# Kernel tuning notes

Measured on AMD Instinct MI355X. Metric: run time of the kernel, lower is better.

The kernel has to match this reference:

```python
import jax, jax.numpy as jnp
import numpy as np

N_QUBITS = 8
N_CYCLES = 4
N_LAYERS = 2  # log2(8) - 1
B = 65536

CNOT = jnp.array([[1, 0, 0, 0],
                  [0, 1, 0, 0],
                  [0, 0, 0, 1],
                  [0, 0, 1, 0]], dtype=jnp.complex64)


def apply_gate(state, U, wires):
    """Apply a (2^k x 2^k) gate U on the given wires of state (B, 2,2,...,2).
    Wire 0 is the leftmost (most significant) qubit axis."""
    k = len(wires)
    src = [w + 1 for w in wires]
    dst = list(range(1, 1 + k))
    st = jnp.moveaxis(state, src, dst)
    shp = st.shape
    st = st.reshape(shp[0], 2 ** k, -1)
    st = jnp.einsum('ij,bjr->bir', U, st)
    return jnp.moveaxis(st.reshape(shp), dst, src)


def apply_ry(state, q, angles):
    """Batched RY(angle) on qubit q; angles has shape (B,)."""
    st = jnp.moveaxis(state, q + 1, 1)  # (B, 2, rest...)
    c = jnp.cos(0.5 * angles).reshape((-1,) + (1,) * (st.ndim - 2))
    s = jnp.sin(0.5 * angles).reshape((-1,) + (1,) * (st.ndim - 2))
    s0, s1 = st[:, 0], st[:, 1]
    new = jnp.stack([c * s0 - s * s1, s * s0 + c * s1], axis=1)
    return jnp.moveaxis(new, 1, q + 1)


def crx_mat(theta):
    c = (jnp.cos(0.5 * theta) + 0j).astype(jnp.complex64)
    s = (-1j * jnp.sin(0.5 * theta)).astype(jnp.complex64)
    one = jnp.ones((), jnp.complex64)
    zero = jnp.zeros((), jnp.complex64)
    return jnp.stack([
        jnp.stack([one, zero, zero, zero]),
        jnp.stack([zero, one, zero, zero]),
        jnp.stack([zero, zero, c, s]),
        jnp.stack([zero, zero, s, c]),
    ])


def u3_mat(p):
    th, ph, lm = p[0], p[1], p[2]
    ct = (jnp.cos(0.5 * th) + 0j).astype(jnp.complex64)
    st = (jnp.sin(0.5 * th) + 0j).astype(jnp.complex64)
    el = jnp.exp(1j * lm).astype(jnp.complex64)
    ep = jnp.exp(1j * ph).astype(jnp.complex64)
    return jnp.stack([
        jnp.stack([ct, -el * st]),
        jnp.stack([ep * st, ep * el * ct]),
    ])


def expval_z(state, q):
    st = jnp.moveaxis(state, q + 1, 1)
    p = (st.real ** 2 + st.imag ** 2).reshape(st.shape[0], 2, -1).sum(-1)
    return p[:, 0] - p[:, 1]


def _forward(x, crx_theta, u3_params, w1, b1, w2, b2):
    b = x.shape[0]
    # |0...0> initial state, shape (B, 2,2,...,2)
    state = jnp.zeros((b, 2 ** N_QUBITS), jnp.complex64).at[:, 0].set(1.0)
    state = state.reshape((b,) + (2,) * N_QUBITS)
    # encoder: data re-uploading RY angle encoding + CNOT ring, n_cycles times
    for _ in range(N_CYCLES):
        for q in range(N_QUBITS):
            state = apply_ry(state, q, x[:, q])
        for q in range(N_QUBITS):
            state = apply_gate(state, CNOT, [q, (q + 1) % N_QUBITS])
    # QCNN conv/pool layers with shared weights per layer
    active = list(range(N_QUBITS))
    for layer in range(N_LAYERS):
        U = crx_mat(crx_theta[layer])
        for i in range(0, len(active) - 1, 2):
            state = apply_gate(state, U, [active[i], active[i + 1]])
        for i in range(1, len(active) - 1, 2):
            state = apply_gate(state, U, [active[i], active[i + 1]])
        remain = active[1::2]
        # mid-circuit expval in the original is discarded and does not alter state
        V = u3_mat(u3_params[layer])
        for q in remain:
            state = apply_gate(state, V, [q])
        active = remain
    feats = jnp.stack([expval_z(state, q) for q in active], axis=1)  # (B, 2)
    h = jnp.tanh(feats @ w1 + b1)
    return jax.nn.sigmoid(h @ w2 + b2)  # (B, 1)


def setup_inputs() -> dict:
    key = jax.random.key(0)
    ks = jax.random.split(key, 6)
    return {
        'x': jax.random.normal(ks[0], (B, N_QUBITS), jnp.float32),
        'crx_theta': jax.random.normal(ks[1], (N_LAYERS,), jnp.float32),
        'u3_params': jax.random.normal(ks[2], (N_LAYERS, 3), jnp.float32),
        'w1': jax.random.normal(ks[3], (2, 10), jnp.float32) * 0.5,
        'b1': jnp.zeros((10,), jnp.float32),
        'w2': jax.random.normal(ks[4], (10, 1), jnp.float32) * 0.5,
        'b2': jnp.zeros((1,), jnp.float32),
    }


def reference(x, crx_theta, u3_params, w1, b1, w2, b2):
    return _forward(x, crx_theta, u3_params, w1, b1, w2, b2)
```

## Files before the change

kernel.cpp:

```cpp
#include <hip/hip_runtime.h>


#define NQ 8

template<int M>
__device__ __forceinline__ float sx(float v) {
    if constexpr (M == 32) return __shfl_xor(v, 32, 64);
    else return __int_as_float(__builtin_amdgcn_ds_swizzle(
                 __float_as_int(v), (M << 10) | 0x1F));
}

__device__ __forceinline__ float bperm(int byte_addr, float v) {
    return __int_as_float(__builtin_amdgcn_ds_bpermute(byte_addr, __float_as_int(v)));
}

#define RY_L(q, M) do { \
    float o0 = sx<M>(a0), o1 = sx<M>(a1), o2 = sx<M>(a2), o3 = sx<M>(a3); \
    a0 = fmaf(c[q], a0, ts[q]*o0); a1 = fmaf(c[q], a1, ts[q]*o1); \
    a2 = fmaf(c[q], a2, ts[q]*o2); a3 = fmaf(c[q], a3, ts[q]*o3); \
} while(0)

#define CNOT_FUSED() do { \
    float t0 = pb ? a2 : a0, t1 = pb ? a3 : a1, t2 = pb ? a1 : a3, t3 = pb ? a0 : a2; \
    a0 = bperm(ba0, t0); a2 = bperm(ba0, t2); \
    a1 = bperm(ba1, t1); a3 = bperm(ba1, t3); \
} while(0)

#define SHFL8(M) \
    float ro0=sx<M>(re0), io0=sx<M>(im0), ro1=sx<M>(re1), io1=sx<M>(im1), \
          ro2=sx<M>(re2), io2=sx<M>(im2), ro3=sx<M>(re3), io3=sx<M>(im3);

#define CRX_LL(CSH, M, cc, sn) do { \
    const bool ct = (l >> (CSH)) & 1; \
    SHFL8(M) \
    if (ct) { \
        re0 = cc*re0 + sn*io0; im0 = cc*im0 - sn*ro0; \
        re1 = cc*re1 + sn*io1; im1 = cc*im1 - sn*ro1; \
        re2 = cc*re2 + sn*io2; im2 = cc*im2 - sn*ro2; \
        re3 = cc*re3 + sn*io3; im3 = cc*im3 - sn*ro3; \
    } \
} while(0)

#define CRX_FIRST_LL(CSH, M, cc, sn) do { \
    const bool ct = (l >> (CSH)) & 1; \
    float ro0 = sx<M>(re0), ro1 = sx<M>(re1), ro2 = sx<M>(re2), ro3 = sx<M>(re3); \
    if (ct) { \
        im0 = -sn*ro0; re0 = cc*re0; \
        im1 = -sn*ro1; re1 = cc*re1; \
        im2 = -sn*ro2; re2 = cc*re2; \
        im3 = -sn*ro3; re3 = cc*re3; \
    } \
} while(0)

#define RYC0(M, T) do { \
    SHFL8(M) \
    re0 = fmaf(uct0, re0, (T)*ro0); im0 = fmaf(uct0, im0, (T)*io0); \
    re1 = fmaf(uct0, re1, (T)*ro1); im1 = fmaf(uct0, im1, (T)*io1); \
    re2 = fmaf(uct0, re2, (T)*ro2); im2 = fmaf(uct0, im2, (T)*io2); \
    re3 = fmaf(uct0, re3, (T)*ro3); im3 = fmaf(uct0, im3, (T)*io3); \
} while(0)

#define DIAG4(CA, SA, CB, SB) do { float r_; \
    r_ = (CA)*re0 - (SA)*im0; im0 = fmaf((CA), im0, (SA)*re0); re0 = r_; \
    r_ = (CB)*re1 - (SB)*im1; im1 = fmaf((CB), im1, (SB)*re1); re1 = r_; \
    r_ = (CA)*re2 - (SA)*im2; im2 = fmaf((CA), im2, (SA)*re2); re2 = r_; \
    r_ = (CB)*re3 - (SB)*im3; im3 = fmaf((CB), im3, (SB)*re3); re3 = r_; \
} while(0)

#define U3D_LANE(SH, M, UCT, UST, CL, SL, CP, SP) do { \
    const bool b = (l >> (SH)) & 1; \
    if (b) { \
        float r; \
        r = CL*re0 - SL*im0; im0 = CL*im0 + SL*re0; re0 = r; \
        r = CL*re1 - SL*im1; im1 = CL*im1 + SL*re1; re1 = r; \
        r = CL*re2 - SL*im2; im2 = CL*im2 + SL*re2; re2 = r; \
        r = CL*re3 - SL*im3; im3 = CL*im3 + SL*re3; re3 = r; \
    } \
    { \
        const float t = b ? (UST) : -(UST); \
        SHFL8(M) \
        re0 = fmaf(UCT, re0, t*ro0); im0 = fmaf(UCT, im0, t*io0); \
        re1 = fmaf(UCT, re1, t*ro1); im1 = fmaf(UCT, im1, t*io1); \
        re2 = fmaf(UCT, re2, t*ro2); im2 = fmaf(UCT, im2, t*io2); \
        re3 = fmaf(UCT, re3, t*ro3); im3 = fmaf(UCT, im3, t*io3); \
    } \
    if (b) { \
        float r; \
        r = CP*re0 - SP*im0; im0 = CP*im0 + SP*re0; re0 = r; \
        r = CP*re1 - SP*im1; im1 = CP*im1 + SP*re1; re1 = r; \
        r = CP*re2 - SP*im2; im2 = CP*im2 + SP*re2; re2 = r; \
        r = CP*re3 - SP*im3; im3 = CP*im3 + SP*re3; re3 = r; \
    } \
} while(0)

#define U3_Q7(CTR, M01R, M01I, M10R, M10I, M11R, M11I) do { \
    float nr0 = CTR*re0 + M01R*re1 - M01I*im1; \
    float ni0 = CTR*im0 + M01R*im1 + M01I*re1; \
    float nr1 = M10R*re0 - M10I*im0 + M11R*re1 - M11I*im1; \
    float ni1 = M10R*im0 + M10I*re0 + M11R*im1 + M11I*re1; \
    float nr2 = CTR*re2 + M01R*re3 - M01I*im3; \
    float ni2 = CTR*im2 + M01R*im3 + M01I*re3; \
    float nr3 = M10R*re2 - M10I*im2 + M11R*re3 - M11I*im3; \
    float ni3 = M10R*im2 + M10I*re2 + M11R*im3 + M11I*re3; \
    re0 = nr0; im0 = ni0; re1 = nr1; im1 = ni1; \
    re2 = nr2; im2 = ni2; re3 = nr3; im3 = ni3; \
} while(0)

__global__ void qcnn_prep(const float* __restrict__ crx,
                          const float* __restrict__ u3p,
                          float* __restrict__ ws) {
    if (threadIdx.x == 0 && blockIdx.x == 0) {
        float sc0, cc0, sc1, cc1;
        __sincosf(0.5f * crx[0], &sc0, &cc0);
        __sincosf(0.5f * crx[1], &sc1, &cc1);
        ws[0] = cc0; ws[1] = sc0; ws[2] = cc1; ws[3] = sc1;
        {
            float th = u3p[0], ph = u3p[1], lm = u3p[2];
            float st_, ct_;
            __sincosf(0.5f * th, &st_, &ct_);
            ws[4] = ct_; ws[5] = st_; ws[6] = lm; ws[7] = ph;
        }
        {
            float th = u3p[3], ph = u3p[4], lm = u3p[5];
            float st_, ct_, sl, cl, sp, cp, spl, cpl;
            __sincosf(0.5f * th, &st_, &ct_);
            __sincosf(lm, &sl, &cl);
            __sincosf(ph, &sp, &cp);
            __sincosf(ph + lm, &spl, &cpl);
            ws[8] = ct_;  ws[9] = st_;  ws[10] = cl; ws[11] = sl; ws[12] = cp; ws[13] = sp;
            ws[14] = -st_ * cl;  ws[15] = -st_ * sl;
            ws[16] =  st_ * cp;  ws[17] =  st_ * sp;
            ws[18] =  ct_ * cpl; ws[19] =  ct_ * spl;
        }
    }
}

__global__ __launch_bounds__(256) void qcnn_kernel(
    const float* __restrict__ x,
    const float* __restrict__ ws,
    const float* __restrict__ w1,
    const float* __restrict__ b1,
    const float* __restrict__ w2,
    const float* __restrict__ b2,
    float* __restrict__ out,
    int Btot)
{
    const int gtid = blockIdx.x * blockDim.x + threadIdx.x;
    const int wave = gtid >> 6;
    const int l = threadIdx.x & 63;
    if (wave >= Btot) return;

    const bool pb = __builtin_popcount(l) & 1;
    const int addr0 = (l & 32) | ((l ^ (l >> 1)) & 31);
    const int ba0 = addr0 << 2;
    const int ba1 = ba0 ^ (48 << 2);

    const float4* xv = (const float4*)(x + wave * NQ);
    float4 xa = xv[0], xb = xv[1];
    float c[NQ], s[NQ], ts[6];
    {
        float ang[NQ] = {xa.x, xa.y, xa.z, xa.w, xb.x, xb.y, xb.z, xb.w};
#pragma unroll
        for (int q = 0; q < NQ; ++q) __sincosf(0.5f * ang[q], &s[q], &c[q]);
#pragma unroll
        for (int q = 0; q < 6; ++q) ts[q] = ((l >> (5 - q)) & 1) ? s[q] : -s[q];
    }

    const float crc0 = ws[0], crs0 = ws[1], crc1 = ws[2], crs1 = ws[3];
    const float uct0 = ws[4], ust0 = ws[5], lm0 = ws[6], ph0 = ws[7];
    const float uct1 = ws[8],  ust1 = ws[9],  cl1 = ws[10], sl1 = ws[11], cp1 = ws[12], sp1 = ws[13];
    const float u01r1 = ws[14], u01i1 = ws[15], u10r1 = ws[16], u10i1 = ws[17], u11r1 = ws[18], u11i1 = ws[19];

    const float kf = (float)(((l >> 4) & 1) + ((l >> 2) & 1) + (l & 1));
    float sA0, cA0, sB0, cB0, sA1, cA1, sB1, cB1;
    __sincosf(kf * lm0,          &sA0, &cA0);
    __sincosf((kf + 1.f) * lm0,  &sB0, &cB0);
    __sincosf(kf * ph0,          &sA1, &cA1);
    __sincosf((kf + 1.f) * ph0,  &sB1, &cB1);
    const float tu1 = ((l >> 4) & 1) ? ust0 : -ust0;
    const float tu3 = ((l >> 2) & 1) ? ust0 : -ust0;
    const float tu5 = (l & 1)        ? ust0 : -ust0;

    float a0, a1, a2, a3;
    {
        float pl = (((l >> 5) & 1) ? s[0] : c[0]);
        pl *= (((l >> 4) & 1) ? s[1] : c[1]);
        pl *= (((l >> 3) & 1) ? s[2] : c[2]);
        pl *= (((l >> 2) & 1) ? s[3] : c[3]);
        pl *= (((l >> 1) & 1) ? s[4] : c[4]);
        pl *= ((l & 1) ? s[5] : c[5]);
        float pc6 = pl * c[6], ps6 = pl * s[6];
        a0 = pc6 * c[7]; a1 = pc6 * s[7];
        a2 = ps6 * c[7]; a3 = ps6 * s[7];
    }
    CNOT_FUSED();
#pragma unroll
    for (int cyc = 0; cyc < 3; ++cyc) {
        RY_L(0, 32); RY_L(1, 16); RY_L(2, 8); RY_L(3, 4); RY_L(4, 2); RY_L(5, 1);
        {
            float n0 = c[6]*a0 - s[6]*a2, n1 = c[6]*a1 - s[6]*a3;
            float n2 = s[6]*a0 + c[6]*a2, n3 = s[6]*a1 + c[6]*a3;
            a0 = n0; a1 = n1; a2 = n2; a3 = n3;
        }
        {
            float n0 = c[7]*a0 - s[7]*a1, n1 = s[7]*a0 + c[7]*a1;
            float n2 = c[7]*a2 - s[7]*a3, n3 = s[7]*a2 + c[7]*a3;
            a0 = n0; a1 = n1; a2 = n2; a3 = n3;
        }
        CNOT_FUSED();
    }

    float re0 = a0, re1 = a1, re2 = a2, re3 = a3;
    float im0 = 0.f, im1 = 0.f, im2 = 0.f, im3 = 0.f;

    CRX_FIRST_LL(5, 16, crc0, crs0);
    CRX_LL(3, 4,  crc0, crs0);
    CRX_LL(1, 1,  crc0, crs0);
    {
        float nr2 = crc0*re2 + crs0*im3, ni2 = crc0*im2 - crs0*re3;
        float nr3 = crc0*re3 + crs0*im2, ni3 = crc0*im3 - crs0*re2;
        re2 = nr2; im2 = ni2; re3 = nr3; im3 = ni3;
    }
    CRX_LL(4, 8, crc0, crs0);
    CRX_LL(2, 2, crc0, crs0);
    {
        if (l & 1) {
            float nr0 = crc0*re0 + crs0*im2, ni0 = crc0*im0 - crs0*re2;
            float nr2 = crc0*re2 + crs0*im0, ni2 = crc0*im2 - crs0*re0;
            float nr1 = crc0*re1 + crs0*im3, ni1 = crc0*im1 - crs0*re3;
            float nr3 = crc0*re3 + crs0*im1, ni3 = crc0*im3 - crs0*re1;
            re0 = nr0; im0 = ni0; re1 = nr1; im1 = ni1;
            re2 = nr2; im2 = ni2; re3 = nr3; im3 = ni3;
        }
    }
    DIAG4(cA0, sA0, cB0, sB0);
    RYC0(16, tu1);
    RYC0(4,  tu3);
    RYC0(1,  tu5);
    {
        float nr0 = uct0*re0 - ust0*re1, ni0 = uct0*im0 - ust0*im1;
        float nr1 = ust0*re0 + uct0*re1, ni1 = ust0*im0 + uct0*im1;
        float nr2 = uct0*re2 - ust0*re3, ni2 = uct0*im2 - ust0*im3;
        float nr3 = ust0*re2 + uct0*re3, ni3 = ust0*im2 + uct0*im3;
        re0 = nr0; im0 = ni0; re1 = nr1; im1 = ni1;
        re2 = nr2; im2 = ni2; re3 = nr3; im3 = ni3;
    }
    DIAG4(cA1, sA1, cB1, sB1);

    CRX_LL(4, 4, crc1, crs1);
    {
        if (l & 1) {
            float nr0 = crc1*re0 + crs1*im1, ni0 = crc1*im0 - crs1*re1;
            float nr1 = crc1*re1 + crs1*im0, ni1 = crc1*im1 - crs1*re0;
            float nr2 = crc1*re2 + crs1*im3, ni2 = crc1*im2 - crs1*re3;
            float nr3 = crc1*re3 + crs1*im2, ni3 = crc1*im3 - crs1*re2;
            re0 = nr0; im0 = ni0; re1 = nr1; im1 = ni1;
            re2 = nr2; im2 = ni2; re3 = nr3; im3 = ni3;
        }
    }
    CRX_LL(2, 1, crc1, crs1);
    U3D_LANE(2, 4, uct1, ust1, cl1, sl1, cp1, sp1);
    U3_Q7(uct1, u01r1, u01i1, u10r1, u10i1, u11r1, u11i1);

    float n0 = re0*re0 + im0*im0;
    float n1 = re1*re1 + im1*im1;
    float n2 = re2*re2 + im2*im2;
    float n3 = re3*re3 + im3*im3;
    float f0 = (((l >> 2) & 1) ? -1.0f : 1.0f) * (n0 + n1 + n2 + n3);
    float f1 = (n0 - n1) + (n2 - n3);
    f0 += sx<1>(f0);  f1 += sx<1>(f1);
    f0 += sx<2>(f0);  f1 += sx<2>(f1);
    f0 += sx<4>(f0);  f1 += sx<4>(f1);
    f0 += sx<8>(f0);  f1 += sx<8>(f1);
    f0 += sx<16>(f0); f1 += sx<16>(f1);
    f0 += sx<32>(f0); f1 += sx<32>(f1);

    const int k = l & 15;
    float contrib = 0.0f;
    if (k < 10) {
        float z = fmaf(f0, w1[k], fmaf(f1, w1[10 + k], b1[k]));
        float e = __expf(2.0f * z);
        float h = (e - 1.0f) / (e + 1.0f);
        contrib = h * w2[k];
    }
    contrib += sx<1>(contrib);
    contrib += sx<2>(contrib);
    contrib += sx<4>(contrib);
    contrib += sx<8>(contrib);
    if (l == 0) {
        float a = contrib + b2[0];
        out[wave] = 1.0f / (1.0f + __expf(-a));
    }
}

extern "C" void kernel_launch(void* const* d_in, const int* in_sizes, int n_in,
                              void* d_out, int out_size, void* d_ws, size_t ws_size,
                              hipStream_t stream) {
    const float* x   = (const float*)d_in[0];
    const float* crx = (const float*)d_in[1];
    const float* u3p = (const float*)d_in[2];
    const float* w1  = (const float*)d_in[3];
    const float* b1  = (const float*)d_in[4];
    const float* w2  = (const float*)d_in[5];
    const float* b2  = (const float*)d_in[6];
    float* out = (float*)d_out;
    float* ws  = (float*)d_ws;

    const int B = in_sizes[0] / NQ;
    hipLaunchKernelGGL(qcnn_prep, dim3(1), dim3(64), 0, stream, crx, u3p, ws);
    const int wavesPerBlock = 256 / 64;
    const int grid = (B + wavesPerBlock - 1) / wavesPerBlock;
    hipLaunchKernelGGL(qcnn_kernel, dim3(grid), dim3(256), 0, stream,
                       x, ws, w1, b1, w2, b2, out, B);
}
```

Measured before the change: 142.0 us.

## Vectorize state arithmetic with packed float2 FMAs and precompute phase table

Rewrites the per-lane amplitude math to use two-wide float vectors so the compiler can emit packed FP32 instructions (v_pk_fma_f32) on CDNA, roughly halving ALU instruction count for gate updates. Separately, moves the per-lane sincos of phase multiples into the prep kernel as a small table indexed by lane popcount, replacing four sincos per lane with two vector loads. Shuffles remain scalar; packed code may add register moves or swizzle overhead for the vector swaps.

```diff
diff --git a/kernel.cpp b/kernel.cpp
--- a/kernel.cpp
+++ b/kernel.cpp
@@ -2,6 +2,12 @@
 
 
 #define NQ 8
+
+typedef float v2 __attribute__((ext_vector_type(2)));
+
+__device__ __forceinline__ v2 sp(float x) { return (v2){x, x}; }
+__device__ __forceinline__ v2 fma2(v2 a, v2 b, v2 c) { return __builtin_elementwise_fma(a, b, c); }
+__device__ __forceinline__ v2 swp(v2 v) { return __builtin_shufflevector(v, v, 1, 0); }
 
 template<int M>
 __device__ __forceinline__ float sx(float v) {
@@ -9,101 +15,42 @@
     else return __int_as_float(__builtin_amdgcn_ds_swizzle(
                  __float_as_int(v), (M << 10) | 0x1F));
 }
-
+template<int M>
+__device__ __forceinline__ v2 sx2(v2 v) {
+    v2 r; r.x = sx<M>(v.x); r.y = sx<M>(v.y); return r;
+}
 __device__ __forceinline__ float bperm(int byte_addr, float v) {
     return __int_as_float(__builtin_amdgcn_ds_bpermute(byte_addr, __float_as_int(v)));
 }
 
 #define RY_L(q, M) do { \
-    float o0 = sx<M>(a0), o1 = sx<M>(a1), o2 = sx<M>(a2), o3 = sx<M>(a3); \
-    a0 = fmaf(c[q], a0, ts[q]*o0); a1 = fmaf(c[q], a1, ts[q]*o1); \
-    a2 = fmaf(c[q], a2, ts[q]*o2); a3 = fmaf(c[q], a3, ts[q]*o3); \
+    v2 oA = sx2<M>(A), oB = sx2<M>(B); \
+    A = fma2(sp(c[q]), A, sp(ts[q]) * oA); \
+    B = fma2(sp(c[q]), B, sp(ts[q]) * oB); \
 } while(0)
 
 #define CNOT_FUSED() do { \
-    float t0 = pb ? a2 : a0, t1 = pb ? a3 : a1, t2 = pb ? a1 : a3, t3 = pb ? a0 : a2; \
-    a0 = bperm(ba0, t0); a2 = bperm(ba0, t2); \
-    a1 = bperm(ba1, t1); a3 = bperm(ba1, t3); \
+    v2 TA = pb ? B : A; \
+    v2 TS = pb ? A : B; \
+    A = (v2){ bperm(ba0, TA.x), bperm(ba1, TA.y) }; \
+    B = (v2){ bperm(ba0, TS.y), bperm(ba1, TS.x) }; \
 } while(0)
-
-#define SHFL8(M) \
-    float ro0=sx<M>(re0), io0=sx<M>(im0), ro1=sx<M>(re1), io1=sx<M>(im1), \
-          ro2=sx<M>(re2), io2=sx<M>(im2), ro3=sx<M>(re3), io3=sx<M>(im3);
 
 #define CRX_LL(CSH, M, cc, sn) do { \
     const bool ct = (l >> (CSH)) & 1; \
-    SHFL8(M) \
+    v2 oRa = sx2<M>(Ra), oIa = sx2<M>(Ia), oRb = sx2<M>(Rb), oIb = sx2<M>(Ib); \
     if (ct) { \
-        re0 = cc*re0 + sn*io0; im0 = cc*im0 - sn*ro0; \
-        re1 = cc*re1 + sn*io1; im1 = cc*im1 - sn*ro1; \
-        re2 = cc*re2 + sn*io2; im2 = cc*im2 - sn*ro2; \
-        re3 = cc*re3 + sn*io3; im3 = cc*im3 - sn*ro3; \
+        Ra = fma2(sp(cc), Ra, sp(sn)  * oIa); \
+        Ia = fma2(sp(cc), Ia, sp(-(sn)) * oRa); \
+        Rb = fma2(sp(cc), Rb, sp(sn)  * oIb); \
+        Ib = fma2(sp(cc), Ib, sp(-(sn)) * oRb); \
     } \
 } while(0)
 
-#define CRX_FIRST_LL(CSH, M, cc, sn) do { \
-    const bool ct = (l >> (CSH)) & 1; \
-    float ro0 = sx<M>(re0), ro1 = sx<M>(re1), ro2 = sx<M>(re2), ro3 = sx<M>(re3); \
-    if (ct) { \
-        im0 = -sn*ro0; re0 = cc*re0; \
-        im1 = -sn*ro1; re1 = cc*re1; \
-        im2 = -sn*ro2; re2 = cc*re2; \
-        im3 = -sn*ro3; re3 = cc*re3; \
-    } \
-} while(0)
-
 #define RYC0(M, T) do { \
-    SHFL8(M) \
-    re0 = fmaf(uct0, re0, (T)*ro0); im0 = fmaf(uct0, im0, (T)*io0); \
-    re1 = fmaf(uct0, re1, (T)*ro1); im1 = fmaf(uct0, im1, (T)*io1); \
-    re2 = fmaf(uct0, re2, (T)*ro2); im2 = fmaf(uct0, im2, (T)*io2); \
-    re3 = fmaf(uct0, re3, (T)*ro3); im3 = fmaf(uct0, im3, (T)*io3); \
-} while(0)
-
-#define DIAG4(CA, SA, CB, SB) do { float r_; \
-    r_ = (CA)*re0 - (SA)*im0; im0 = fmaf((CA), im0, (SA)*re0); re0 = r_; \
-    r_ = (CB)*re1 - (SB)*im1; im1 = fmaf((CB), im1, (SB)*re1); re1 = r_; \
-    r_ = (CA)*re2 - (SA)*im2; im2 = fmaf((CA), im2, (SA)*re2); re2 = r_; \
-    r_ = (CB)*re3 - (SB)*im3; im3 = fmaf((CB), im3, (SB)*re3); re3 = r_; \
-} while(0)
-
-#define U3D_LANE(SH, M, UCT, UST, CL, SL, CP, SP) do { \
-    const bool b = (l >> (SH)) & 1; \
-    if (b) { \
-        float r; \
-        r = CL*re0 - SL*im0; im0 = CL*im0 + SL*re0; re0 = r; \
-        r = CL*re1 - SL*im1; im1 = CL*im1 + SL*re1; re1 = r; \
-        r = CL*re2 - SL*im2; im2 = CL*im2 + SL*re2; re2 = r; \
-        r = CL*re3 - SL*im3; im3 = CL*im3 + SL*re3; re3 = r; \
-    } \
-    { \
-        const float t = b ? (UST) : -(UST); \
-        SHFL8(M) \
-        re0 = fmaf(UCT, re0, t*ro0); im0 = fmaf(UCT, im0, t*io0); \
-        re1 = fmaf(UCT, re1, t*ro1); im1 = fmaf(UCT, im1, t*io1); \
-        re2 = fmaf(UCT, re2, t*ro2); im2 = fmaf(UCT, im2, t*io2); \
-        re3 = fmaf(UCT, re3, t*ro3); im3 = fmaf(UCT, im3, t*io3); \
-    } \
-    if (b) { \
-        float r; \
-        r = CP*re0 - SP*im0; im0 = CP*im0 + SP*re0; re0 = r; \
-        r = CP*re1 - SP*im1; im1 = CP*im1 + SP*re1; re1 = r; \
-        r = CP*re2 - SP*im2; im2 = CP*im2 + SP*re2; re2 = r; \
-        r = CP*re3 - SP*im3; im3 = CP*im3 + SP*re3; re3 = r; \
-    } \
-} while(0)
-
-#define U3_Q7(CTR, M01R, M01I, M10R, M10I, M11R, M11I) do { \
-    float nr0 = CTR*re0 + M01R*re1 - M01I*im1; \
-    float ni0 = CTR*im0 + M01R*im1 + M01I*re1; \
-    float nr1 = M10R*re0 - M10I*im0 + M11R*re1 - M11I*im1; \
-    float ni1 = M10R*im0 + M10I*re0 + M11R*im1 + M11I*re1; \
-    float nr2 = CTR*re2 + M01R*re3 - M01I*im3; \
-    float ni2 = CTR*im2 + M01R*im3 + M01I*re3; \
-    float nr3 = M10R*re2 - M10I*im2 + M11R*re3 - M11I*im3; \
-    float ni3 = M10R*im2 + M10I*re2 + M11R*im3 + M11I*re3; \
-    re0 = nr0; im0 = ni0; re1 = nr1; im1 = ni1; \
-    re2 = nr2; im2 = ni2; re3 = nr3; im3 = ni3; \
+    v2 oRa = sx2<M>(Ra), oIa = sx2<M>(Ia), oRb = sx2<M>(Rb), oIb = sx2<M>(Ib); \
+    Ra = fma2(sp(uct0), Ra, sp(T) * oRa); Ia = fma2(sp(uct0), Ia, sp(T) * oIa); \
+    Rb = fma2(sp(uct0), Rb, sp(T) * oRb); Ib = fma2(sp(uct0), Ib, sp(T) * oIb); \
 } while(0)
 
 __global__ void qcnn_prep(const float* __restrict__ crx,
@@ -114,23 +61,35 @@
         __sincosf(0.5f * crx[0], &sc0, &cc0);
         __sincosf(0.5f * crx[1], &sc1, &cc1);
         ws[0] = cc0; ws[1] = sc0; ws[2] = cc1; ws[3] = sc1;
+        float lm0, ph0;
         {
-            float th = u3p[0], ph = u3p[1], lm = u3p[2];
+            float th = u3p[0]; ph0 = u3p[1]; lm0 = u3p[2];
             float st_, ct_;
             __sincosf(0.5f * th, &st_, &ct_);
-            ws[4] = ct_; ws[5] = st_; ws[6] = lm; ws[7] = ph;
+            ws[4] = ct_; ws[5] = st_;
         }
         {
             float th = u3p[3], ph = u3p[4], lm = u3p[5];
-            float st_, ct_, sl, cl, sp, cp, spl, cpl;
+            float st_, ct_, sl, cl, sp_, cp, spl, cpl;
             __sincosf(0.5f * th, &st_, &ct_);
             __sincosf(lm, &sl, &cl);
-            __sincosf(ph, &sp, &cp);
+            __sincosf(ph, &sp_, &cp);
             __sincosf(ph + lm, &spl, &cpl);
-            ws[8] = ct_;  ws[9] = st_;  ws[10] = cl; ws[11] = sl; ws[12] = cp; ws[13] = sp;
+            ws[8] = ct_;  ws[9] = st_;  ws[10] = cl; ws[11] = sl; ws[12] = cp; ws[13] = sp_;
             ws[14] = -st_ * cl;  ws[15] = -st_ * sl;
-            ws[16] =  st_ * cp;  ws[17] =  st_ * sp;
+            ws[16] =  st_ * cp;  ws[17] =  st_ * sp_;
             ws[18] =  ct_ * cpl; ws[19] =  ct_ * spl;
+        }
+        for (int k = 0; k < 4; ++k) {
+            float kf = (float)k;
+            float sA0, cA0, sB0, cB0, sA1, cA1, sB1, cB1;
+            __sincosf(kf * lm0,         &sA0, &cA0);
+            __sincosf((kf + 1.f) * lm0, &sB0, &cB0);
+            __sincosf(kf * ph0,         &sA1, &cA1);
+            __sincosf((kf + 1.f) * ph0, &sB1, &cB1);
+            float* q = ws + 20 + k * 8;
+            q[0] = cA0; q[1] = sA0; q[2] = cB0; q[3] = sB0;
+            q[4] = cA1; q[5] = sA1; q[6] = cB1; q[7] = sB1;
         }
     }
 }
@@ -167,21 +126,20 @@
     }
 
     const float crc0 = ws[0], crs0 = ws[1], crc1 = ws[2], crs1 = ws[3];
-    const float uct0 = ws[4], ust0 = ws[5], lm0 = ws[6], ph0 = ws[7];
+    const float uct0 = ws[4], ust0 = ws[5];
     const float uct1 = ws[8],  ust1 = ws[9],  cl1 = ws[10], sl1 = ws[11], cp1 = ws[12], sp1 = ws[13];
     const float u01r1 = ws[14], u01i1 = ws[15], u10r1 = ws[16], u10i1 = ws[17], u11r1 = ws[18], u11i1 = ws[19];
 
-    const float kf = (float)(((l >> 4) & 1) + ((l >> 2) & 1) + (l & 1));
-    float sA0, cA0, sB0, cB0, sA1, cA1, sB1, cB1;
-    __sincosf(kf * lm0,          &sA0, &cA0);
-    __sincosf((kf + 1.f) * lm0,  &sB0, &cB0);
-    __sincosf(kf * ph0,          &sA1, &cA1);
-    __sincosf((kf + 1.f) * ph0,  &sB1, &cB1);
+    const int ki = ((l >> 4) & 1) + ((l >> 2) & 1) + (l & 1);
+    const float4* dtab = (const float4*)(ws + 20 + ki * 8);
+    float4 d0 = dtab[0], d1 = dtab[1];
+    const v2 CAB_lm = {d0.x, d0.z}, SAB_lm = {d0.y, d0.w};
+    const v2 CAB_ph = {d1.x, d1.z}, SAB_ph = {d1.y, d1.w};
     const float tu1 = ((l >> 4) & 1) ? ust0 : -ust0;
     const float tu3 = ((l >> 2) & 1) ? ust0 : -ust0;
     const float tu5 = (l & 1)        ? ust0 : -ust0;
 
-    float a0, a1, a2, a3;
+    v2 A, B;
     {
         float pl = (((l >> 5) & 1) ? s[0] : c[0]);
         pl *= (((l >> 4) & 1) ? s[1] : c[1]);
@@ -189,96 +147,136 @@
         pl *= (((l >> 2) & 1) ? s[3] : c[3]);
         pl *= (((l >> 1) & 1) ? s[4] : c[4]);
         pl *= ((l & 1) ? s[5] : c[5]);
-        float pc6 = pl * c[6], ps6 = pl * s[6];
-        a0 = pc6 * c[7]; a1 = pc6 * s[7];
-        a2 = ps6 * c[7]; a3 = ps6 * s[7];
+        v2 cs7 = {c[7], s[7]};
+        A = sp(pl * c[6]) * cs7;
+        B = sp(pl * s[6]) * cs7;
     }
     CNOT_FUSED();
 #pragma unroll
     for (int cyc = 0; cyc < 3; ++cyc) {
         RY_L(0, 32); RY_L(1, 16); RY_L(2, 8); RY_L(3, 4); RY_L(4, 2); RY_L(5, 1);
         {
-            float n0 = c[6]*a0 - s[6]*a2, n1 = c[6]*a1 - s[6]*a3;
-            float n2 = s[6]*a0 + c[6]*a2, n3 = s[6]*a1 + c[6]*a3;
-            a0 = n0; a1 = n1; a2 = n2; a3 = n3;
+            v2 nA = fma2(sp(-s[6]), B, sp(c[6]) * A);
+            B = fma2(sp(c[6]), B, sp(s[6]) * A);
+            A = nA;
         }
         {
-            float n0 = c[7]*a0 - s[7]*a1, n1 = s[7]*a0 + c[7]*a1;
-            float n2 = c[7]*a2 - s[7]*a3, n3 = s[7]*a2 + c[7]*a3;
-            a0 = n0; a1 = n1; a2 = n2; a3 = n3;
+            v2 sv = {-s[7], s[7]};
+            A = fma2(sp(c[7]), A, sv * swp(A));
+            B = fma2(sp(c[7]), B, sv * swp(B));
         }
         CNOT_FUSED();
     }
 
-    float re0 = a0, re1 = a1, re2 = a2, re3 = a3;
-    float im0 = 0.f, im1 = 0.f, im2 = 0.f, im3 = 0.f;
-
-    CRX_FIRST_LL(5, 16, crc0, crs0);
-    CRX_LL(3, 4,  crc0, crs0);
-    CRX_LL(1, 1,  crc0, crs0);
-    {
-        float nr2 = crc0*re2 + crs0*im3, ni2 = crc0*im2 - crs0*re3;
-        float nr3 = crc0*re3 + crs0*im2, ni3 = crc0*im3 - crs0*re2;
-        re2 = nr2; im2 = ni2; re3 = nr3; im3 = ni3;
+    v2 Ra = A, Rb = B, Ia = sp(0.f), Ib = sp(0.f);
+
+    {
+        const bool ct = (l >> 5) & 1;
+        v2 oRa = sx2<16>(Ra), oRb = sx2<16>(Rb);
+        if (ct) {
+            Ia = sp(-crs0) * oRa; Ra = sp(crc0) * Ra;
+            Ib = sp(-crs0) * oRb; Rb = sp(crc0) * Rb;
+        }
+    }
+    CRX_LL(3, 4, crc0, crs0);
+    CRX_LL(1, 1, crc0, crs0);
+    {
+        v2 nRb = fma2(sp(crc0), Rb, sp(crs0) * swp(Ib));
+        Ib = fma2(sp(crc0), Ib, sp(-crs0) * swp(Rb));
+        Rb = nRb;
     }
     CRX_LL(4, 8, crc0, crs0);
     CRX_LL(2, 2, crc0, crs0);
     {
         if (l & 1) {
-            float nr0 = crc0*re0 + crs0*im2, ni0 = crc0*im0 - crs0*re2;
-            float nr2 = crc0*re2 + crs0*im0, ni2 = crc0*im2 - crs0*re0;
-            float nr1 = crc0*re1 + crs0*im3, ni1 = crc0*im1 - crs0*re3;
-            float nr3 = crc0*re3 + crs0*im1, ni3 = crc0*im3 - crs0*re1;
-            re0 = nr0; im0 = ni0; re1 = nr1; im1 = ni1;
-            re2 = nr2; im2 = ni2; re3 = nr3; im3 = ni3;
-        }
-    }
-    DIAG4(cA0, sA0, cB0, sB0);
+            v2 nRa = fma2(sp(crc0), Ra, sp(crs0) * Ib);
+            v2 nRb = fma2(sp(crc0), Rb, sp(crs0) * Ia);
+            v2 nIa = fma2(sp(crc0), Ia, sp(-crs0) * Rb);
+            v2 nIb = fma2(sp(crc0), Ib, sp(-crs0) * Ra);
+            Ra = nRa; Rb = nRb; Ia = nIa; Ib = nIb;
+        }
+    }
+    {
+        v2 nRa = fma2(CAB_lm, Ra, -SAB_lm * Ia);
+        Ia = fma2(CAB_lm, Ia, SAB_lm * Ra); Ra = nRa;
+        v2 nRb = fma2(CAB_lm, Rb, -SAB_lm * Ib);
+        Ib = fma2(CAB_lm, Ib, SAB_lm * Rb); Rb = nRb;
+    }
     RYC0(16, tu1);
     RYC0(4,  tu3);
     RYC0(1,  tu5);
     {
-        float nr0 = uct0*re0 - ust0*re1, ni0 = uct0*im0 - ust0*im1;
-        float nr1 = ust0*re0 + uct0*re1, ni1 = ust0*im0 + uct0*im1;
-        float nr2 = uct0*re2 - ust0*re3, ni2 = uct0*im2 - ust0*im3;
-        float nr3 = ust0*re2 + uct0*re3, ni3 = ust0*im2 + uct0*im3;
-        re0 = nr0; im0 = ni0; re1 = nr1; im1 = ni1;
-        re2 = nr2; im2 = ni2; re3 = nr3; im3 = ni3;
-    }
-    DIAG4(cA1, sA1, cB1, sB1);
+        v2 usv = {-ust0, ust0};
+        Ra = fma2(sp(uct0), Ra, usv * swp(Ra));
+        Rb = fma2(sp(uct0), Rb, usv * swp(Rb));
+        Ia = fma2(sp(uct0), Ia, usv * swp(Ia));
+        Ib = fma2(sp(uct0), Ib, usv * swp(Ib));
+    }
+    {
+        v2 nRa = fma2(CAB_ph, Ra, -SAB_ph * Ia);
+        Ia = fma2(CAB_ph, Ia, SAB_ph * Ra); Ra = nRa;
+        v2 nRb = fma2(CAB_ph, Rb, -SAB_ph * Ib);
+        Ib = fma2(CAB_ph, Ib, SAB_ph * Rb); Rb = nRb;
+    }
 
     CRX_LL(4, 4, crc1, crs1);
     {
         if (l & 1) {
-            float nr0 = crc1*re0 + crs1*im1, ni0 = crc1*im0 - crs1*re1;
-            float nr1 = crc1*re1 + crs1*im0, ni1 = crc1*im1 - crs1*re0;
-            float nr2 = crc1*re2 + crs1*im3, ni2 = crc1*im2 - crs1*re3;
-            float nr3 = crc1*re3 + crs1*im2, ni3 = crc1*im3 - crs1*re2;
-            re0 = nr0; im0 = ni0; re1 = nr1; im1 = ni1;
-            re2 = nr2; im2 = ni2; re3 = nr3; im3 = ni3;
+            v2 nRa = fma2(sp(crc1), Ra, sp(crs1) * swp(Ia));
+            v2 nIa = fma2(sp(crc1), Ia, sp(-crs1) * swp(Ra));
+            v2 nRb = fma2(sp(crc1), Rb, sp(crs1) * swp(Ib));
+            v2 nIb = fma2(sp(crc1), Ib, sp(-crs1) * swp(Rb));
+            Ra = nRa; Ia = nIa; Rb = nRb; Ib = nIb;
         }
     }
     CRX_LL(2, 1, crc1, crs1);
-    U3D_LANE(2, 4, uct1, ust1, cl1, sl1, cp1, sp1);
-    U3_Q7(uct1, u01r1, u01i1, u10r1, u10i1, u11r1, u11i1);
-
-    float n0 = re0*re0 + im0*im0;
-    float n1 = re1*re1 + im1*im1;
-    float n2 = re2*re2 + im2*im2;
-    float n3 = re3*re3 + im3*im3;
-    float f0 = (((l >> 2) & 1) ? -1.0f : 1.0f) * (n0 + n1 + n2 + n3);
-    float f1 = (n0 - n1) + (n2 - n3);
-    f0 += sx<1>(f0);  f1 += sx<1>(f1);
-    f0 += sx<2>(f0);  f1 += sx<2>(f1);
-    f0 += sx<4>(f0);  f1 += sx<4>(f1);
-    f0 += sx<8>(f0);  f1 += sx<8>(f1);
-    f0 += sx<16>(f0); f1 += sx<16>(f1);
-    f0 += sx<32>(f0); f1 += sx<32>(f1);
+    {
+        const bool b = (l >> 2) & 1;
+        if (b) {
+            v2 nRa = fma2(sp(cl1), Ra, sp(-sl1) * Ia);
+            Ia = fma2(sp(cl1), Ia, sp(sl1) * Ra); Ra = nRa;
+            v2 nRb = fma2(sp(cl1), Rb, sp(-sl1) * Ib);
+            Ib = fma2(sp(cl1), Ib, sp(sl1) * Rb); Rb = nRb;
+        }
+        const float t = b ? ust1 : -ust1;
+        v2 oRa = sx2<4>(Ra), oIa = sx2<4>(Ia), oRb = sx2<4>(Rb), oIb = sx2<4>(Ib);
+        Ra = fma2(sp(uct1), Ra, sp(t) * oRa); Ia = fma2(sp(uct1), Ia, sp(t) * oIa);
+        Rb = fma2(sp(uct1), Rb, sp(t) * oRb); Ib = fma2(sp(uct1), Ib, sp(t) * oIb);
+        if (b) {
+            v2 nRa = fma2(sp(cp1), Ra, sp(-sp1) * Ia);
+            Ia = fma2(sp(cp1), Ia, sp(sp1) * Ra); Ra = nRa;
+            v2 nRb = fma2(sp(cp1), Rb, sp(-sp1) * Ib);
+            Ib = fma2(sp(cp1), Ib, sp(sp1) * Rb); Rb = nRb;
+        }
+    }
+    {
+        v2 E0 = {uct1, u11r1}, E1 = {u01r1, u10r1};
+        v2 E2 = {0.f, -u11i1}, E3 = {-u01i1, -u10i1};
+        v2 G2 = {0.f,  u11i1}, G3 = { u01i1,  u10i1};
+        v2 sRa = swp(Ra), sIa = swp(Ia), sRb = swp(Rb), sIb = swp(Ib);
+        v2 nRa = fma2(E3, sIa, fma2(E2, Ia, fma2(E1, sRa, E0 * Ra)));
+        v2 nIa = fma2(G3, sRa, fma2(G2, Ra, fma2(E1, sIa, E0 * Ia)));
+        v2 nRb = fma2(E3, sIb, fma2(E2, Ib, fma2(E1, sRb, E0 * Rb)));
+        v2 nIb = fma2(G3, sRb, fma2(G2, Rb, fma2(E1, sIb, E0 * Ib)));
+        Ra = nRa; Ia = nIa; Rb = nRb; Ib = nIb;
+    }
+
+    v2 Na = fma2(Ia, Ia, Ra * Ra);
+    v2 Nb = fma2(Ib, Ib, Rb * Rb);
+    v2 T = Na + Nb;
+    const float sgn = ((l >> 2) & 1) ? -1.0f : 1.0f;
+    v2 F = { sgn * (T.x + T.y), T.x - T.y };
+    F += sx2<1>(F);
+    F += sx2<2>(F);
+    F += sx2<4>(F);
+    F += sx2<8>(F);
+    F += sx2<16>(F);
+    F += sx2<32>(F);
 
     const int k = l & 15;
     float contrib = 0.0f;
     if (k < 10) {
-        float z = fmaf(f0, w1[k], fmaf(f1, w1[10 + k], b1[k]));
+        float z = fmaf(F.x, w1[k], fmaf(F.y, w1[10 + k], b1[k]));
         float e = __expf(2.0f * z);
         float h = (e - 1.0f) / (e + 1.0f);
         contrib = h * w2[k];
```

New measurement: 128.6 us. 9.4% less time.
